# Performance work log

Measured on AMD Instinct MI355X. Metric: run time of the kernel, lower is better.

## Reference

```python
import jax, jax.numpy as jnp
import numpy as np

B, T, D, C = 16, 1500, 768, 1024

def setup_inputs() -> dict:
    key = jax.random.key(0)
    k1, k2 = jax.random.split(key)
    embed = jax.random.normal(k1, (B, T, D), dtype=jnp.float32)
    cluster_centers = jax.random.normal(k2, (C, D), dtype=jnp.float32)
    return {"embed": embed, "cluster_centers": cluster_centers}

def reference(embed, cluster_centers):
    # Faithful to: dists = -torch.cdist(embed, centers, p=2); clusters = dists.argmax(-1)
    # Euclidean distance via ||e||^2 - 2 e.c + ||c||^2 (GEMM-friendly form).
    e_sq = jnp.sum(embed * embed, axis=-1, keepdims=True)            # (b, t, 1)
    c_sq = jnp.sum(cluster_centers * cluster_centers, axis=-1)       # (c,)
    cross = jnp.einsum('btd,cd->btc', embed, cluster_centers)        # (b, t, c)
    d2 = jnp.maximum(e_sq - 2.0 * cross + c_sq, 0.0)
    dists = -jnp.sqrt(d2)                                            # negative L2 distance
    clusters = jnp.argmax(dists, axis=-1)                            # (b, t) int
    return clusters
```

## Files before the change

### kernel.cpp

```cpp
#include <hip/hip_runtime.h>
#include <cstdint>
#include <cstddef>

#define MROWS 24000
#define NCOLS 1024
#define KDIM  768
#define MT 188
#define KT 48
#define NT 4

typedef _Float16 f16x8  __attribute__((ext_vector_type(8)));
typedef float    f32x16 __attribute__((ext_vector_type(16)));

typedef __attribute__((address_space(1))) void as1_void;
typedef __attribute__((address_space(3))) void as3_void;

#define A_BYTES   (188ull*48*8192)
#define B_OFF     A_BYTES
#define B_BYTES   (4ull*48*16384)
#define CH_OFF    (A_BYTES + B_BYTES)
#define PART_OFF  (CH_OFF + 4096)
#define WS_NEED   (PART_OFF + 24064ull*4*8)

__global__ void k_tile_A(const float* __restrict__ E, _Float16* __restrict__ Aw) {
  int bid = blockIdx.x;
  int mt = bid / 48, kt = bid % 48;
  int t = threadIdx.x;
  int r = t >> 1, p = t & 1;
  int row = mt * 128 + r;
  __shared__ _Float16 lh[2][128][8];
  __shared__ _Float16 ll[2][128][8];
  float x[8];
  if (row < MROWS) {
    const float4* s4 = (const float4*)(E + (size_t)row * KDIM + kt * 16 + p * 8);
    float4 v0 = s4[0], v1 = s4[1];
    x[0]=v0.x; x[1]=v0.y; x[2]=v0.z; x[3]=v0.w; x[4]=v1.x; x[5]=v1.y; x[6]=v1.z; x[7]=v1.w;
  } else {
#pragma unroll
    for (int e = 0; e < 8; ++e) x[e] = 0.f;
  }
#pragma unroll
  for (int e = 0; e < 8; ++e) {
    _Float16 h = (_Float16)x[e];
    lh[p][r][e] = h;
    ll[p][r][e] = (_Float16)(x[e] - (float)h);
  }
  __syncthreads();
  const uint4* sh = (const uint4*)&lh[0][0][0];
  const uint4* sl = (const uint4*)&ll[0][0][0];
  uint4* dst = (uint4*)(Aw + (size_t)bid * 4096);
  dst[t]       = sh[t];
  dst[256 + t] = sl[t];
}

__global__ void k_tile_B(const float* __restrict__ C, _Float16* __restrict__ Bw) {
  int bid = blockIdx.x;
  int nt = bid / 48, kt = bid % 48;
  int t = threadIdx.x;
  int c = t >> 1, p = t & 1;
  __shared__ _Float16 lh[2][256][8];
  __shared__ _Float16 ll[2][256][8];
  const float4* s4 = (const float4*)(C + (size_t)(nt * 256 + c) * KDIM + kt * 16 + p * 8);
  float4 v0 = s4[0], v1 = s4[1];
  float x[8] = {v0.x, v0.y, v0.z, v0.w, v1.x, v1.y, v1.z, v1.w};
#pragma unroll
  for (int e = 0; e < 8; ++e) {
    _Float16 h = (_Float16)x[e];
    lh[p][c][e] = h;
    ll[p][c][e] = (_Float16)(x[e] - (float)h);
  }
  __syncthreads();
  const uint4* sh = (const uint4*)&lh[0][0][0];
  const uint4* sl = (const uint4*)&ll[0][0][0];
  uint4* dst = (uint4*)(Bw + (size_t)bid * 8192);
  dst[t]       = sh[t];
  dst[512 + t] = sl[t];
}

__global__ void k_chalf(const float* __restrict__ C, float* __restrict__ ch) {
  int c = blockIdx.x, t = threadIdx.x;
  const float* src = C + (size_t)c * KDIM;
  float sq = 0.f;
#pragma unroll
  for (int i = 0; i < 3; ++i) {
    float x = src[t + i * 256];
    sq = fmaf(x, x, sq);
  }
#pragma unroll
  for (int m = 1; m < 64; m <<= 1) sq += __shfl_xor(sq, m, 64);
  __shared__ float part[4];
  if ((t & 63) == 0) part[t >> 6] = sq;
  __syncthreads();
  if (t == 0) ch[c] = 0.5f * ((part[0] + part[1]) + (part[2] + part[3]));
}

#define MFMA16(a, b, c) __builtin_amdgcn_mfma_f32_32x32x16_f16((a), (b), (c), 0, 0, 0)

__global__ __launch_bounds__(512, 4) void k_gemm(
    const _Float16* __restrict__ Aw, const _Float16* __restrict__ Bw,
    const float* __restrict__ ch, uint2* __restrict__ part) {
  __shared__ __align__(16) char smem[3][8192];
  __shared__ float red_v[4][128];
  __shared__ int   red_i[4][128];

  const int bid0 = blockIdx.x;
  const int swz = (bid0 & 7) * 94 + (bid0 >> 3);
  const int nt = swz / MT, mt = swz % MT;

  const int tid = threadIdx.x, lane = tid & 63, wid = tid >> 6;
  const int wm = wid >> 2, wn = wid & 3;
  const int lo5 = lane & 31, p = lane >> 5;

  const char* Ab = (const char*)Aw + (size_t)mt * (48 * 8192);
  const char* Bb = (const char*)Bw + (size_t)nt * (48 * 16384);

  auto stageA = [&](char* sb, int kt) {
    __builtin_amdgcn_global_load_lds((as1_void*)(Ab + kt * 8192 + tid * 16),
                                     (as3_void*)(sb + tid * 16), 16, 0, 0);
  };

  f32x16 acc[2][2] = {};
  const int offA = p * 2048 + (wm * 64 + lo5) * 16;
  const int offB = p * 4096 + (wn * 64 + lo5) * 16;

  f16x8 bh0, bh1, bl0, bl1;
  auto loadB = [&](int kt) {
    const char* gb = Bb + (size_t)kt * 16384;
    bh0 = *(const f16x8*)(gb + offB);
    bh1 = *(const f16x8*)(gb + offB + 512);
    bl0 = *(const f16x8*)(gb + 8192 + offB);
    bl1 = *(const f16x8*)(gb + 8192 + offB + 512);
  };

  stageA(smem[0], 0);
  stageA(smem[1], 1);
  loadB(0);

  auto ktile = [&](const char* rb, char* wb, int j) {
    asm volatile("s_waitcnt vmcnt(5)" ::: "memory");
    __builtin_amdgcn_s_barrier();
    f16x8 ah0 = *(const f16x8*)(rb + offA);
    f16x8 ah1 = *(const f16x8*)(rb + offA + 512);
    f16x8 al0 = *(const f16x8*)(rb + 4096 + offA);
    f16x8 al1 = *(const f16x8*)(rb + 4096 + offA + 512);
    __builtin_amdgcn_s_setprio(1);
    acc[0][0] = MFMA16(ah0, bh0, acc[0][0]);
    acc[0][0] = MFMA16(ah0, bl0, acc[0][0]);
    acc[0][0] = MFMA16(al0, bh0, acc[0][0]);
    acc[1][0] = MFMA16(ah1, bh0, acc[1][0]);
    acc[1][0] = MFMA16(ah1, bl0, acc[1][0]);
    acc[1][0] = MFMA16(al1, bh0, acc[1][0]);
    acc[0][1] = MFMA16(ah0, bh1, acc[0][1]);
    acc[0][1] = MFMA16(ah0, bl1, acc[0][1]);
    acc[0][1] = MFMA16(al0, bh1, acc[0][1]);
    acc[1][1] = MFMA16(ah1, bh1, acc[1][1]);
    acc[1][1] = MFMA16(ah1, bl1, acc[1][1]);
    acc[1][1] = MFMA16(al1, bh1, acc[1][1]);
    __builtin_amdgcn_s_setprio(0);
    if (j + 2 < KT) stageA(wb, j + 2);
    if (j + 1 < KT) loadB(j + 1);
  };

  for (int j = 0; j < KT; j += 3) {
    ktile(smem[0], smem[2], j);
    ktile(smem[1], smem[0], j + 1);
    ktile(smem[2], smem[1], j + 2);
  }

  int c0 = nt * 256 + wn * 64 + lo5;
  int c1 = c0 + 32;
  float ch0 = ch[c0];
  float ch1 = ch[c1];
#pragma unroll
  for (int mi = 0; mi < 2; ++mi)
#pragma unroll
    for (int q = 0; q < 16; ++q) {
      float s0 = acc[mi][0][q] - ch0;
      float s1 = acc[mi][1][q] - ch1;
      float v = s0; int ix = c0;
      if (s1 > v) { v = s1; ix = c1; }
#pragma unroll
      for (int m = 1; m <= 16; m <<= 1) {
        float ov = __shfl_xor(v, m, 64);
        int   oi = __shfl_xor(ix, m, 64);
        if (ov > v || (ov == v && oi < ix)) { v = ov; ix = oi; }
      }
      if (lo5 == 0) {
        int rr = (q & 3) + ((q >> 2) << 3) + (p << 2);
        int rloc = wm * 64 + mi * 32 + rr;
        red_v[wn][rloc] = v;
        red_i[wn][rloc] = ix;
      }
    }
  __syncthreads();
  if (tid < 128) {
    float v = red_v[0][tid];
    int ix = red_i[0][tid];
#pragma unroll
    for (int w = 1; w < 4; ++w) {
      float ov = red_v[w][tid];
      int oi = red_i[w][tid];
      if (ov > v) { v = ov; ix = oi; }
    }
    int rowg = mt * 128 + tid;
    part[rowg * 4 + nt] = uint2{ __float_as_uint(v), (unsigned)ix };
  }
}

__global__ void k_merge(const uint2* __restrict__ part, int* __restrict__ out) {
  int r = blockIdx.x * 256 + threadIdx.x;
  if (r >= MROWS) return;
  uint2 b0 = part[r * 4];
  float bvv = __uint_as_float(b0.x);
  int bii = (int)b0.y;
#pragma unroll
  for (int j = 1; j < 4; ++j) {
    uint2 pj = part[r * 4 + j];
    float v = __uint_as_float(pj.x);
    if (v > bvv) { bvv = v; bii = (int)pj.y; }
  }
  out[r] = bii;
}

__global__ void k_naive(const float* __restrict__ E, const float* __restrict__ C,
                        int* __restrict__ out) {
  int row = blockIdx.x * 4 + (threadIdx.x >> 6);
  int lane = threadIdx.x & 63;
  const float* e = E + (size_t)row * KDIM;
  float bvv = -3.4e38f;
  int bii = 0;
  for (int c = 0; c < NCOLS; ++c) {
    const float* cc = C + (size_t)c * KDIM;
    float dot = 0.f, csq = 0.f;
    for (int d = lane; d < KDIM; d += 64) {
      float cv = cc[d];
      dot = fmaf(e[d], cv, dot);
      csq = fmaf(cv, cv, csq);
    }
#pragma unroll
    for (int m = 1; m < 64; m <<= 1) {
      dot += __shfl_xor(dot, m, 64);
      csq += __shfl_xor(csq, m, 64);
    }
    float s = dot - 0.5f * csq;
    if (s > bvv) { bvv = s; bii = c; }
  }
  if (lane == 0) out[row] = bii;
}

extern "C" void kernel_launch(void* const* d_in, const int* in_sizes, int n_in,
                              void* d_out, int out_size, void* d_ws, size_t ws_size,
                              hipStream_t stream) {
  const float* embed   = (const float*)d_in[0];
  const float* centers = (const float*)d_in[1];
  int* out = (int*)d_out;

  if (ws_size >= WS_NEED) {
    char* w = (char*)d_ws;
    _Float16* Aw = (_Float16*)w;
    _Float16* Bw = (_Float16*)(w + B_OFF);
    float*    ch = (float*)(w + CH_OFF);
    uint2*  partb = (uint2*)(w + PART_OFF);
    k_tile_A<<<188 * 48, 256, 0, stream>>>(embed, Aw);
    k_tile_B<<<4 * 48, 512, 0, stream>>>(centers, Bw);
    k_chalf<<<1024, 256, 0, stream>>>(centers, ch);
    k_gemm<<<752, 512, 0, stream>>>(Aw, Bw, ch, partb);
    k_merge<<<94, 256, 0, stream>>>(partb, out);
  } else {
    k_naive<<<6000, 256, 0, stream>>>(embed, centers, out);
  }
}
```

Measured before the change: 176.5 us.

## Load GEMM A and B fragments directly from global memory without LDS pipeline

Removes the triple-buffered LDS staging of A tiles (global_load_lds with waitcnt/barrier) and the software prefetch of B, replacing them with a simple non-unrolled loop that loads both A and B fragments straight from global memory each k-step. This drops barriers, LDS usage and priority hints, which may raise occupancy and cut synchronization overhead. It also loses the overlap of loads with MFMA work, and A fragments shared across the four wn warps are now fetched redundantly from global/cache instead of once into LDS.

```diff
diff --git a/kernel.cpp b/kernel.cpp
--- a/kernel.cpp
+++ b/kernel.cpp
@@ -99,7 +99,6 @@
 __global__ __launch_bounds__(512, 4) void k_gemm(
     const _Float16* __restrict__ Aw, const _Float16* __restrict__ Bw,
     const float* __restrict__ ch, uint2* __restrict__ part) {
-  __shared__ __align__(16) char smem[3][8192];
   __shared__ float red_v[4][128];
   __shared__ int   red_i[4][128];
 
@@ -114,36 +113,23 @@
   const char* Ab = (const char*)Aw + (size_t)mt * (48 * 8192);
   const char* Bb = (const char*)Bw + (size_t)nt * (48 * 16384);
 
-  auto stageA = [&](char* sb, int kt) {
-    __builtin_amdgcn_global_load_lds((as1_void*)(Ab + kt * 8192 + tid * 16),
-                                     (as3_void*)(sb + tid * 16), 16, 0, 0);
-  };
-
-  f32x16 acc[2][2] = {};
   const int offA = p * 2048 + (wm * 64 + lo5) * 16;
   const int offB = p * 4096 + (wn * 64 + lo5) * 16;
 
-  f16x8 bh0, bh1, bl0, bl1;
-  auto loadB = [&](int kt) {
-    const char* gb = Bb + (size_t)kt * 16384;
-    bh0 = *(const f16x8*)(gb + offB);
-    bh1 = *(const f16x8*)(gb + offB + 512);
-    bl0 = *(const f16x8*)(gb + 8192 + offB);
-    bl1 = *(const f16x8*)(gb + 8192 + offB + 512);
-  };
-
-  stageA(smem[0], 0);
-  stageA(smem[1], 1);
-  loadB(0);
-
-  auto ktile = [&](const char* rb, char* wb, int j) {
-    asm volatile("s_waitcnt vmcnt(5)" ::: "memory");
-    __builtin_amdgcn_s_barrier();
-    f16x8 ah0 = *(const f16x8*)(rb + offA);
-    f16x8 ah1 = *(const f16x8*)(rb + offA + 512);
-    f16x8 al0 = *(const f16x8*)(rb + 4096 + offA);
-    f16x8 al1 = *(const f16x8*)(rb + 4096 + offA + 512);
-    __builtin_amdgcn_s_setprio(1);
+  f32x16 acc[2][2] = {};
+
+#pragma unroll 1
+  for (int kt = 0; kt < KT; ++kt) {
+    const char* ga = Ab + kt * 8192;
+    const char* gb = Bb + kt * 16384;
+    f16x8 ah0 = *(const f16x8*)(ga + offA);
+    f16x8 ah1 = *(const f16x8*)(ga + offA + 512);
+    f16x8 al0 = *(const f16x8*)(ga + 4096 + offA);
+    f16x8 al1 = *(const f16x8*)(ga + 4096 + offA + 512);
+    f16x8 bh0 = *(const f16x8*)(gb + offB);
+    f16x8 bh1 = *(const f16x8*)(gb + offB + 512);
+    f16x8 bl0 = *(const f16x8*)(gb + 8192 + offB);
+    f16x8 bl1 = *(const f16x8*)(gb + 8192 + offB + 512);
     acc[0][0] = MFMA16(ah0, bh0, acc[0][0]);
     acc[0][0] = MFMA16(ah0, bl0, acc[0][0]);
     acc[0][0] = MFMA16(al0, bh0, acc[0][0]);
@@ -156,15 +142,6 @@
     acc[1][1] = MFMA16(ah1, bh1, acc[1][1]);
     acc[1][1] = MFMA16(ah1, bl1, acc[1][1]);
     acc[1][1] = MFMA16(al1, bh1, acc[1][1]);
-    __builtin_amdgcn_s_setprio(0);
-    if (j + 2 < KT) stageA(wb, j + 2);
-    if (j + 1 < KT) loadB(j + 1);
-  };
-
-  for (int j = 0; j < KT; j += 3) {
-    ktile(smem[0], smem[2], j);
-    ktile(smem[1], smem[0], j + 1);
-    ktile(smem[2], smem[1], j + 2);
   }
 
   int c0 = nt * 256 + wn * 64 + lo5;
```

Result: slower. 184.6 us (+4.6%).

## Widen GEMM tile to 512 columns and stage B through LDS

Applied to the files above, without the earlier changes.

Each GEMM block now covers 128 rows by 512 cluster columns using 1024 threads (16 waves), so the A tile is reused across twice as many columns and only 376 blocks are launched. B fragments are no longer read by each wave straight from global memory. They are staged into triple-buffered LDS with global_load_lds next to A, which cuts redundant B traffic. The merge pass now combines two partials per row instead of four. In exchange, LDS use per block grows to about 120KB and there are fewer blocks, which may limit occupancy and latency hiding on the 256 CUs.

```diff
diff --git a/kernel.cpp b/kernel.cpp
--- a/kernel.cpp
+++ b/kernel.cpp
@@ -7,7 +7,7 @@
 #define KDIM  768
 #define MT 188
 #define KT 48
-#define NT 4
+#define NT 2
 
 typedef _Float16 f16x8  __attribute__((ext_vector_type(8)));
 typedef float    f32x16 __attribute__((ext_vector_type(16)));
@@ -96,53 +96,55 @@
 
 #define MFMA16(a, b, c) __builtin_amdgcn_mfma_f32_32x32x16_f16((a), (b), (c), 0, 0, 0)
 
-__global__ __launch_bounds__(512, 4) void k_gemm(
+__global__ __launch_bounds__(1024, 4) void k_gemm(
     const _Float16* __restrict__ Aw, const _Float16* __restrict__ Bw,
     const float* __restrict__ ch, uint2* __restrict__ part) {
-  __shared__ __align__(16) char smem[3][8192];
-  __shared__ float red_v[4][128];
-  __shared__ int   red_i[4][128];
+  __shared__ __align__(16) char smem[3][40960];
+  __shared__ float red_v[8][128];
+  __shared__ int   red_i[8][128];
 
   const int bid0 = blockIdx.x;
-  const int swz = (bid0 & 7) * 94 + (bid0 >> 3);
+  const int swz = (bid0 & 7) * 47 + (bid0 >> 3);
   const int nt = swz / MT, mt = swz % MT;
 
   const int tid = threadIdx.x, lane = tid & 63, wid = tid >> 6;
-  const int wm = wid >> 2, wn = wid & 3;
+  const int wm = wid >> 3, wn = wid & 7;
   const int lo5 = lane & 31, p = lane >> 5;
 
-  const char* Ab = (const char*)Aw + (size_t)mt * (48 * 8192);
-  const char* Bb = (const char*)Bw + (size_t)nt * (48 * 16384);
-
-  auto stageA = [&](char* sb, int kt) {
-    __builtin_amdgcn_global_load_lds((as1_void*)(Ab + kt * 8192 + tid * 16),
-                                     (as3_void*)(sb + tid * 16), 16, 0, 0);
+  const char* Ab  = (const char*)Aw + (size_t)mt * (48 * 8192);
+  const char* Bb0 = (const char*)Bw + (size_t)(nt * 2 + 0) * (48 * 16384);
+  const char* Bb1 = (const char*)Bw + (size_t)(nt * 2 + 1) * (48 * 16384);
+
+  auto stage = [&](char* sb, int kt) {
+    __builtin_amdgcn_global_load_lds((as1_void*)(Ab + kt * 8192 + (tid & 511) * 16),
+                                     (as3_void*)(sb + (tid & 511) * 16), 16, 0, 0);
+    __builtin_amdgcn_global_load_lds((as1_void*)(Bb0 + (size_t)kt * 16384 + tid * 16),
+                                     (as3_void*)(sb + 8192 + tid * 16), 16, 0, 0);
+    __builtin_amdgcn_global_load_lds((as1_void*)(Bb1 + (size_t)kt * 16384 + tid * 16),
+                                     (as3_void*)(sb + 24576 + tid * 16), 16, 0, 0);
   };
 
   f32x16 acc[2][2] = {};
   const int offA = p * 2048 + (wm * 64 + lo5) * 16;
-  const int offB = p * 4096 + (wn * 64 + lo5) * 16;
-
-  f16x8 bh0, bh1, bl0, bl1;
-  auto loadB = [&](int kt) {
-    const char* gb = Bb + (size_t)kt * 16384;
-    bh0 = *(const f16x8*)(gb + offB);
-    bh1 = *(const f16x8*)(gb + offB + 512);
-    bl0 = *(const f16x8*)(gb + 8192 + offB);
-    bl1 = *(const f16x8*)(gb + 8192 + offB + 512);
-  };
-
-  stageA(smem[0], 0);
-  stageA(smem[1], 1);
-  loadB(0);
+  const int offB = 8192 + (wn >> 2) * 16384 + p * 4096
+                 + ((wn & 3) * 64 + lo5) * 16;
+
+  stage(smem[0], 0);
+  stage(smem[1], 1);
 
   auto ktile = [&](const char* rb, char* wb, int j) {
-    asm volatile("s_waitcnt vmcnt(5)" ::: "memory");
+    if (j < KT - 1) asm volatile("s_waitcnt vmcnt(3)" ::: "memory");
+    else            asm volatile("s_waitcnt vmcnt(0)" ::: "memory");
     __builtin_amdgcn_s_barrier();
     f16x8 ah0 = *(const f16x8*)(rb + offA);
     f16x8 ah1 = *(const f16x8*)(rb + offA + 512);
     f16x8 al0 = *(const f16x8*)(rb + 4096 + offA);
     f16x8 al1 = *(const f16x8*)(rb + 4096 + offA + 512);
+    f16x8 bh0 = *(const f16x8*)(rb + offB);
+    f16x8 bh1 = *(const f16x8*)(rb + offB + 512);
+    f16x8 bl0 = *(const f16x8*)(rb + 8192 + offB);
+    f16x8 bl1 = *(const f16x8*)(rb + 8192 + offB + 512);
+    if (j + 2 < KT) stage(wb, j + 2);
     __builtin_amdgcn_s_setprio(1);
     acc[0][0] = MFMA16(ah0, bh0, acc[0][0]);
     acc[0][0] = MFMA16(ah0, bl0, acc[0][0]);
@@ -157,8 +159,6 @@
     acc[1][1] = MFMA16(ah1, bl1, acc[1][1]);
     acc[1][1] = MFMA16(al1, bh1, acc[1][1]);
     __builtin_amdgcn_s_setprio(0);
-    if (j + 2 < KT) stageA(wb, j + 2);
-    if (j + 1 < KT) loadB(j + 1);
   };
 
   for (int j = 0; j < KT; j += 3) {
@@ -167,7 +167,7 @@
     ktile(smem[2], smem[1], j + 2);
   }
 
-  int c0 = nt * 256 + wn * 64 + lo5;
+  int c0 = nt * 512 + wn * 64 + lo5;
   int c1 = c0 + 32;
   float ch0 = ch[c0];
   float ch1 = ch[c1];
@@ -197,28 +197,25 @@
     float v = red_v[0][tid];
     int ix = red_i[0][tid];
 #pragma unroll
-    for (int w = 1; w < 4; ++w) {
+    for (int w = 1; w < 8; ++w) {
       float ov = red_v[w][tid];
       int oi = red_i[w][tid];
       if (ov > v) { v = ov; ix = oi; }
     }
     int rowg = mt * 128 + tid;
-    part[rowg * 4 + nt] = uint2{ __float_as_uint(v), (unsigned)ix };
+    part[rowg * 2 + nt] = uint2{ __float_as_uint(v), (unsigned)ix };
   }
 }
 
 __global__ void k_merge(const uint2* __restrict__ part, int* __restrict__ out) {
   int r = blockIdx.x * 256 + threadIdx.x;
   if (r >= MROWS) return;
-  uint2 b0 = part[r * 4];
+  uint2 b0 = part[r * 2];
   float bvv = __uint_as_float(b0.x);
   int bii = (int)b0.y;
-#pragma unroll
-  for (int j = 1; j < 4; ++j) {
-    uint2 pj = part[r * 4 + j];
-    float v = __uint_as_float(pj.x);
-    if (v > bvv) { bvv = v; bii = (int)pj.y; }
-  }
+  uint2 p1 = part[r * 2 + 1];
+  float v1 = __uint_as_float(p1.x);
+  if (v1 > bvv) { bvv = v1; bii = (int)p1.y; }
   out[r] = bii;
 }
 
@@ -264,7 +261,7 @@
     k_tile_A<<<188 * 48, 256, 0, stream>>>(embed, Aw);
     k_tile_B<<<4 * 48, 512, 0, stream>>>(centers, Bw);
     k_chalf<<<1024, 256, 0, stream>>>(centers, ch);
-    k_gemm<<<752, 512, 0, stream>>>(Aw, Bw, ch, partb);
+    k_gemm<<<376, 1024, 0, stream>>>(Aw, Bw, ch, partb);
     k_merge<<<94, 256, 0, stream>>>(partb, out);
   } else {
     k_naive<<<6000, 256, 0, stream>>>(embed, centers, out);
```

Result: slower. 198.2 us (+12.3%).
